# Kernel tuning notes

Hardware: AMD Instinct MI355X
Metric: run time of the kernel (lower is better)

Reference implementation:

```python
import jax, jax.numpy as jnp
import numpy as np

PATCH_SIZE = 128
IMG = 256


def _circle_perimeter(r_o, c_o, radius):
    # skimage.draw.circle_perimeter, method='bresenham' (midpoint circle),
    # including the duplicate octant-boundary points that skimage emits.
    rr, cc = [], []
    c, r = 0, radius
    d = 3 - 2 * radius
    while c <= r:
        rr += [r, -r, r, -r, c, -c, c, -c]
        cc += [c, c, -c, -c, r, r, -r, -r]
        if d < 0:
            d += 4 * c + 6
        else:
            d += 4 * (c - r) + 10
            r -= 1
        c += 1
    return np.asarray(rr) + r_o, np.asarray(cc) + c_o


def _radial_indices(patch_size, img):
    cy, cx = img // 2, img // 2
    rr_all, cc_all, seg_all = [], [], []
    for radius in range(1, patch_size - 1):  # radii 1..patch_size-2
        rr, cc = _circle_perimeter(cy, cx, radius)
        rr_all.append(rr)
        cc_all.append(cc)
        seg_all.append(np.full(rr.shape[0], radius - 1))
    return (np.concatenate(rr_all).astype(np.int32),
            np.concatenate(cc_all).astype(np.int32),
            np.concatenate(seg_all).astype(np.int32))


def setup_inputs() -> dict:
    key = jax.random.key(0)
    k1, k2 = jax.random.split(key)
    inp = jax.random.normal(k1, (64, 3, IMG, IMG), dtype=jnp.float32)
    tgt = jax.random.normal(k2, (64, 3, IMG, IMG), dtype=jnp.float32)
    w = np.float32(np.arange(0, 1, 1 / (PATCH_SIZE - 1)))  # length 127
    weights = jnp.asarray(w / np.sum(w))
    rr_idx, cc_idx, seg_ids = _radial_indices(PATCH_SIZE, IMG)
    return {"input": inp, "target": tgt, "weights": weights,
            "rr_idx": jnp.asarray(rr_idx), "cc_idx": jnp.asarray(cc_idx),
            "seg_ids": jnp.asarray(seg_ids)}


def reference(input, target, weights, rr_idx, cc_idx, seg_ids):
    B, C = input.shape[0], input.shape[1]
    R = weights.shape[0]          # patch_size - 1 curve bins
    nseg = R - 1                  # radii 1..patch_size-2
    f1 = jnp.fft.fft2(input)      # complex64 [B,C,H,W]
    f2 = jnp.fft.fft2(target)
    p1 = f1[:, :, rr_idx, cc_idx]  # [B,C,Ntot]
    p2 = f2[:, :, rr_idx, cc_idx]
    # original sums num/den over ALL dims (batch+channel+perimeter points)
    cross = jnp.sum(p1 * jnp.conj(p2), axis=(0, 1))        # [Ntot] complex
    pw1 = jnp.sum(jnp.abs(p1) ** 2, axis=(0, 1))           # [Ntot]
    pw2 = jnp.sum(jnp.abs(p2) ** 2, axis=(0, 1))
    num = jnp.abs(jax.ops.segment_sum(cross, seg_ids, num_segments=nseg))
    den = (jax.ops.segment_sum(pw1, seg_ids, num_segments=nseg) *
           jax.ops.segment_sum(pw2, seg_ids, num_segments=nseg))
    curve = jnp.concatenate([jnp.ones((1,), jnp.float32),
                             (num / jnp.sqrt(den)).astype(jnp.float32)])  # [R]
    # curve is identical across (b, c); Linear(R,1,bias=False) then total sum
    curve_full = jnp.broadcast_to(curve, (B, C, R))
    return jnp.sum(curve_full @ weights)
```

## Files before the change

### kernel.cpp

```cpp
#include <hip/hip_runtime.h>
#include <hip/hip_fp16.h>
#include <math.h>

#define NSEG 126

__device__ __forceinline__ unsigned bitrev8(unsigned v) { return __brev(v) >> 24; }

template <int K>
__device__ __forceinline__ void fftK(float2 x[][4], int lane) {
    const float PI = 3.14159265358979323846f;
    {
        float s, c;
        __sincosf(-PI * (float)lane * (1.0f / 128.0f), &s, &c);
        #pragma unroll
        for (int k = 0; k < K; k++) {
            float2 u, t, d;
            u = x[k][0]; t = x[k][2];
            x[k][0] = make_float2(u.x + t.x, u.y + t.y);
            d = make_float2(u.x - t.x, u.y - t.y);
            x[k][2] = make_float2(d.x * c - d.y * s, d.x * s + d.y * c);
            u = x[k][1]; t = x[k][3];
            x[k][1] = make_float2(u.x + t.x, u.y + t.y);
            d = make_float2(u.x - t.x, u.y - t.y);
            x[k][3] = make_float2(d.x * s + d.y * c, -d.x * c + d.y * s);
        }
    }
    {
        float s, c;
        __sincosf(-PI * (float)lane * (1.0f / 64.0f), &s, &c);
        #pragma unroll
        for (int k = 0; k < K; k++) {
            float2 u, t, d;
            u = x[k][0]; t = x[k][1];
            x[k][0] = make_float2(u.x + t.x, u.y + t.y);
            d = make_float2(u.x - t.x, u.y - t.y);
            x[k][1] = make_float2(d.x * c - d.y * s, d.x * s + d.y * c);
            u = x[k][2]; t = x[k][3];
            x[k][2] = make_float2(u.x + t.x, u.y + t.y);
            d = make_float2(u.x - t.x, u.y - t.y);
            x[k][3] = make_float2(d.x * c - d.y * s, d.x * s + d.y * c);
        }
    }
    #pragma unroll
    for (int hbit = 5; hbit >= 0; hbit--) {
        int h = 1 << hbit;
        int j = lane & (h - 1);
        float s, c;
        __sincosf(-PI * (float)j / (float)h, &s, &c);
        bool up = (lane & h) != 0;
        #pragma unroll
        for (int k = 0; k < K; k++) {
            #pragma unroll
            for (int i = 0; i < 4; i++) {
                float px = __shfl_xor(x[k][i].x, h);
                float py = __shfl_xor(x[k][i].y, h);
                if (up) {
                    float dx = px - x[k][i].x, dy = py - x[k][i].y;
                    x[k][i] = make_float2(dx * c - dy * s, dx * s + dy * c);
                } else {
                    x[k][i] = make_float2(x[k][i].x + px, x[k][i].y + py);
                }
            }
        }
    }
}

__global__ __launch_bounds__(1024) void prep_all(
    const int* __restrict__ rr, const int* __restrict__ cc,
    const int* __restrict__ seg, int n,
    int* __restrict__ starts, int* __restrict__ b_pack, float* __restrict__ acc)
{
    __shared__ int cnt[128];
    __shared__ int cur[128];
    int tid = threadIdx.x;
    if (tid < NSEG * 3) acc[tid] = 0.f;
    if (tid < 128) cnt[tid] = 0;
    __syncthreads();
    for (int i = tid; i < n; i += 1024) {
        int c = cc[i], r = rr[i];
        if ((c > 128) || (c == 128 && r > 128)) atomicAdd(&cnt[255 - c], 1);
    }
    __syncthreads();
    if (tid < 64) {
        int2 c2 = reinterpret_cast<const int2*>(cnt)[tid];
        int lsum = c2.x + c2.y;
        int pre = lsum;
        #pragma unroll
        for (int off = 1; off < 64; off <<= 1) {
            int v = __shfl_up(pre, off);
            if (tid >= off) pre += v;
        }
        int excl = pre - lsum;
        int2 outv = make_int2(excl, excl + c2.x);
        reinterpret_cast<int2*>(cur)[tid] = outv;
        reinterpret_cast<int2*>(starts)[tid] = outv;
        if (tid == 63) starts[128] = excl + c2.x + c2.y;
    }
    __syncthreads();
    for (int i = tid; i < n; i += 1024) {
        int c = cc[i], r = rr[i];
        if ((c > 128) || (c == 128 && r > 128)) {
            int j = 255 - c;
            int pos = atomicAdd(&cur[j], 1);
            int pr = (int)bitrev8((unsigned)r);
            int pm = (int)bitrev8((unsigned)(256 - r) & 255);
            b_pack[pos] = pr | (pm << 8) | (seg[i] << 16);
        }
    }
}

__global__ __launch_bounds__(512) void rowfft_kernel(
    const float* __restrict__ inp, const float* __restrict__ tgt,
    __half2* __restrict__ G, int pair_base)
{
    __shared__ float2 T[256 * 17];
    int bid    = blockIdx.x;
    int plocal = bid >> 4;
    int rowgrp = bid & 15;
    int wv     = threadIdx.x >> 6;
    int lane   = threadIdx.x & 63;
    size_t base = (((size_t)(pair_base + plocal)) << 16)
                + ((size_t)((rowgrp << 4) + (wv << 1)) << 8);
    const float* s1 = inp + base;
    const float* s2 = tgt + base;

    float2 x[2][4];
    #pragma unroll
    for (int k = 0; k < 2; k++)
        #pragma unroll
        for (int i = 0; i < 4; i++) {
            int e = (k << 8) + i * 64 + lane;
            x[k][i] = make_float2(s1[e], s2[e]);
        }
    fftK<2>(x, lane);

    #pragma unroll
    for (int k = 0; k < 2; k++)
        #pragma unroll
        for (int i = 0; i < 4; i++)
            T[(i * 64 + lane) * 17 + (wv << 1) + k] = x[k][i];
    __syncthreads();

    __half2* dst = G + (((size_t)plocal) << 16) + (rowgrp << 4);
    int xl = threadIdx.x & 15;
    int qb = threadIdx.x >> 4;
    #pragma unroll
    for (int ii = 0; ii < 8; ii++) {
        int q = qb + (ii << 5);
        float2 v = T[q * 17 + xl];
        dst[q * 256 + xl] = __float22half2_rn(v);
    }
}

__global__ __launch_bounds__(256) void colfft_gather_kernel(
    const __half2* __restrict__ G, const int* __restrict__ starts,
    const int* __restrict__ b_pack, float* __restrict__ acc)
{
    __shared__ float2 Fb[4][2][256];
    __shared__ float accl[NSEG * 3];
    int tid    = threadIdx.x;
    int wv     = tid >> 6;
    int lane   = tid & 63;
    int plocal = blockIdx.x >> 4;
    int b      = blockIdx.x & 15;
    int jbase  = (b << 3) + (wv << 1);

    for (int i = tid; i < NSEG * 3; i += 256) accl[i] = 0.f;
    __syncthreads();

    const __half2* Gp = G + (((size_t)plocal) << 16);
    int cols[4];
    cols[0] = jbase + 1;   cols[1] = 255 - jbase;
    cols[2] = jbase + 2;   cols[3] = 254 - jbase;

    __half2 h[4][4];
    #pragma unroll
    for (int k = 0; k < 4; k++) {
        int q = (int)bitrev8((unsigned)cols[k]);
        const __half2* col = Gp + ((size_t)q << 8);
        #pragma unroll
        for (int i = 0; i < 4; i++) h[k][i] = col[i * 64 + lane];
    }
    float2 x[4][4];
    #pragma unroll
    for (int k = 0; k < 4; k++)
        #pragma unroll
        for (int i = 0; i < 4; i++)
            x[k][i] = __half22float2(h[k][i]);

    fftK<4>(x, lane);

    float2* F_lo = &Fb[wv][0][0];
    float2* F_hi = &Fb[wv][1][0];
    #pragma unroll
    for (int kb = 0; kb < 2; kb++) {
        #pragma unroll
        for (int i = 0; i < 4; i++) {
            F_lo[i * 64 + lane] = x[2 * kb + 0][i];
            F_hi[i * 64 + lane] = x[2 * kb + 1][i];
        }
        int j = jbase + kb;
        int s0 = starts[j], s1 = starts[j + 1];
        int e  = s0 + lane;
        int pk = (e < s1) ? b_pack[e] : 0;
        while (e < s1) {
            int e2  = e + 64;
            int pk2 = (e2 < s1) ? b_pack[e2] : 0;
            float2 a = F_hi[pk & 255];
            float2 m = F_lo[(pk >> 8) & 255];
            int sg = pk >> 16;
            float f1x = a.x + m.x, f1y = a.y - m.y;
            float dx  = a.x - m.x, dy  = a.y + m.y;
            atomicAdd(&accl[sg * 3 + 0], f1x * dy - f1y * dx);
            atomicAdd(&accl[sg * 3 + 1], f1x * f1x + f1y * f1y);
            atomicAdd(&accl[sg * 3 + 2], dx * dx + dy * dy);
            e = e2; pk = pk2;
        }
    }
    __syncthreads();

    for (int i = tid; i < NSEG * 3; i += 256) {
        float v = accl[i];
        if (v != 0.f) atomicAdd(&acc[i], v);
    }
}

__global__ void final_kernel(const float* __restrict__ acc, const float* __restrict__ w,
                             float* __restrict__ out, float scale) {
    int lane = threadIdx.x;
    float val = 0.f;
    for (int s = lane; s < NSEG; s += 64) {
        float cr = acc[s * 3 + 0];
        float p1 = acc[s * 3 + 1];
        float p2 = acc[s * 3 + 2];
        float den = p1 * p2;
        float curve = den > 0.f ? fabsf(cr) * rsqrtf(den) : 0.f;
        val += curve * w[s + 1];
    }
    if (lane == 0) val += w[0];
    #pragma unroll
    for (int off = 32; off > 0; off >>= 1) val += __shfl_down(val, off);
    if (lane == 0) out[0] = scale * val;
}

extern "C" void kernel_launch(void* const* d_in, const int* in_sizes, int n_in,
                              void* d_out, int out_size, void* d_ws, size_t ws_size,
                              hipStream_t stream)
{
    const float* inp = (const float*)d_in[0];
    const float* tgt = (const float*)d_in[1];
    const float* wts = (const float*)d_in[2];
    const int*   rr  = (const int*)d_in[3];
    const int*   cc  = (const int*)d_in[4];
    const int*   sg  = (const int*)d_in[5];
    int npts   = in_sizes[3];
    int npairs = in_sizes[0] >> 16;

    char* ws = (char*)d_ws;
    float* acc    = (float*)(ws + 0);
    int*   starts = (int*)(ws + 2048);
    int*   b_pack = (int*)(ws + 4096);
    size_t goff = 4096 + (size_t)npts * 4;
    goff = (goff + 255) & ~(size_t)255;
    __half2* G = (__half2*)(ws + goff);

    size_t per_pair = (size_t)256 * 256 * sizeof(__half2);
    int maxchunk = (int)((ws_size > goff ? (ws_size - goff) : 0) / per_pair);
    if (maxchunk < 1) maxchunk = 1;
    if (maxchunk > npairs) maxchunk = npairs;

    prep_all<<<1, 1024, 0, stream>>>(rr, cc, sg, npts, starts, b_pack, acc);

    for (int pb = 0; pb < npairs; pb += maxchunk) {
        int cp = npairs - pb < maxchunk ? npairs - pb : maxchunk;
        rowfft_kernel<<<cp * 16, 512, 0, stream>>>(inp, tgt, G, pb);
        colfft_gather_kernel<<<cp * 16, 256, 0, stream>>>(G, starts, b_pack, acc);
    }

    final_kernel<<<1, 64, 0, stream>>>(acc, wts, (float*)d_out, (float)npairs);
}
```

Baseline: 236.4 us.

## Fuse row FFT, column FFT and gather into one LDS-resident kernel

Replaces the separate row-FFT and column-FFT+gather kernels, which exchanged a half-precision spectrum through global memory, with a single kernel per image pair and half-spectrum. Each block row-FFTs with float4 loads and a new shuffle-based radix schedule using constant twiddle steps, keeps only the 128 needed column bins transposed in LDS as half2, column-FFTs them in place, then gathers perimeter points straight from LDS. This removes the global round trip of the intermediate spectrum and the extra launches. In exchange, each block redoes every row FFT for both halves and uses a large LDS footprint, which lowers occupancy to about one block per CU.

```diff
diff --git a/kernel.cpp b/kernel.cpp
--- a/kernel.cpp
+++ b/kernel.cpp
@@ -3,15 +3,85 @@
 #include <math.h>
 
 #define NSEG 126
+#define PI_F 3.14159265358979323846f
+#define TLS 257
 
 __device__ __forceinline__ unsigned bitrev8(unsigned v) { return __brev(v) >> 24; }
+__device__ __forceinline__ unsigned bitrev6(unsigned v) { return __brev(v) >> 26; }
+__device__ __forceinline__ float2 cmulc(float2 a, float2 b) {
+    return make_float2(a.x*b.x - a.y*b.y, a.x*b.y + a.y*b.x);
+}
+__device__ __forceinline__ float2 mulmi(float2 a){ return make_float2(a.y, -a.x); }
+
+template <int K>
+__device__ __forceinline__ void stage_shfl(float2 x[][4], int lane, int hl,
+                                           float2 w0, float2 st1, float2 st2, float2 st3)
+{
+    float2 w1 = cmulc(w0, st1), w2 = cmulc(w0, st2), w3 = cmulc(w0, st3);
+    bool up = (lane & hl) != 0;
+    #pragma unroll
+    for (int k = 0; k < K; k++) {
+        #pragma unroll
+        for (int i = 0; i < 4; i++) {
+            float2 wi = (i == 0) ? w0 : (i == 1) ? w1 : (i == 2) ? w2 : w3;
+            float px = __shfl_xor(x[k][i].x, hl);
+            float py = __shfl_xor(x[k][i].y, hl);
+            if (up) {
+                float dx = px - x[k][i].x, dy = py - x[k][i].y;
+                x[k][i] = make_float2(dx*wi.x - dy*wi.y, dx*wi.y + dy*wi.x);
+            } else {
+                x[k][i] = make_float2(x[k][i].x + px, x[k][i].y + py);
+            }
+        }
+    }
+}
+
+template <int K>
+__device__ __forceinline__ void fft256_v2(float2 x[][4], int lane) {
+    { float s,c; __sincosf(-PI_F*(float)(lane&31)*(1.0f/32.0f), &s,&c);
+      stage_shfl<K>(x,lane,32, make_float2(c,s),
+        make_float2(0.99969882f,-0.02454123f),
+        make_float2(0.99879546f,-0.04906767f),
+        make_float2(0.99729046f,-0.07356456f)); }
+    { float s,c; __sincosf(-PI_F*(float)(lane&15)*(1.0f/16.0f), &s,&c);
+      stage_shfl<K>(x,lane,16, make_float2(c,s),
+        make_float2(0.99879546f,-0.04906767f),
+        make_float2(0.99518473f,-0.09801714f),
+        make_float2(0.98917651f,-0.14673047f)); }
+    { float s,c; __sincosf(-PI_F*(float)(lane&7)*(1.0f/8.0f), &s,&c);
+      stage_shfl<K>(x,lane,8, make_float2(c,s),
+        make_float2(0.99518473f,-0.09801714f),
+        make_float2(0.98078528f,-0.19509032f),
+        make_float2(0.95694034f,-0.29028468f)); }
+    { float s,c; __sincosf(-PI_F*(float)(lane&3)*(1.0f/4.0f), &s,&c);
+      stage_shfl<K>(x,lane,4, make_float2(c,s),
+        make_float2(0.98078528f,-0.19509032f),
+        make_float2(0.92387953f,-0.38268343f),
+        make_float2(0.83146961f,-0.55557023f)); }
+    { float2 w0 = (lane&1) ? make_float2(0.f,-1.f) : make_float2(1.f,0.f);
+      stage_shfl<K>(x,lane,2, w0,
+        make_float2(0.92387953f,-0.38268343f),
+        make_float2(0.70710678f,-0.70710678f),
+        make_float2(0.38268343f,-0.92387953f)); }
+    { stage_shfl<K>(x,lane,1, make_float2(1.f,0.f),
+        make_float2(0.70710678f,-0.70710678f),
+        make_float2(0.f,-1.f),
+        make_float2(-0.70710678f,-0.70710678f)); }
+    #pragma unroll
+    for (int k = 0; k < K; k++) {
+        float2 u, v;
+        u=x[k][0]; v=x[k][2]; x[k][0]=make_float2(u.x+v.x,u.y+v.y); x[k][2]=make_float2(u.x-v.x,u.y-v.y);
+        u=x[k][1]; v=x[k][3]; x[k][1]=make_float2(u.x+v.x,u.y+v.y); x[k][3]=mulmi(make_float2(u.x-v.x,u.y-v.y));
+        u=x[k][0]; v=x[k][1]; x[k][0]=make_float2(u.x+v.x,u.y+v.y); x[k][1]=make_float2(u.x-v.x,u.y-v.y);
+        u=x[k][2]; v=x[k][3]; x[k][2]=make_float2(u.x+v.x,u.y+v.y); x[k][3]=make_float2(u.x-v.x,u.y-v.y);
+    }
+}
 
 template <int K>
 __device__ __forceinline__ void fftK(float2 x[][4], int lane) {
-    const float PI = 3.14159265358979323846f;
     {
         float s, c;
-        __sincosf(-PI * (float)lane * (1.0f / 128.0f), &s, &c);
+        __sincosf(-PI_F * (float)lane * (1.0f / 128.0f), &s, &c);
         #pragma unroll
         for (int k = 0; k < K; k++) {
             float2 u, t, d;
@@ -27,7 +97,7 @@
     }
     {
         float s, c;
-        __sincosf(-PI * (float)lane * (1.0f / 64.0f), &s, &c);
+        __sincosf(-PI_F * (float)lane * (1.0f / 64.0f), &s, &c);
         #pragma unroll
         for (int k = 0; k < K; k++) {
             float2 u, t, d;
@@ -46,7 +116,7 @@
         int h = 1 << hbit;
         int j = lane & (h - 1);
         float s, c;
-        __sincosf(-PI * (float)j / (float)h, &s, &c);
+        __sincosf(-PI_F * (float)j / (float)h, &s, &c);
         bool up = (lane & h) != 0;
         #pragma unroll
         for (int k = 0; k < K; k++) {
@@ -102,126 +172,110 @@
         if ((c > 128) || (c == 128 && r > 128)) {
             int j = 255 - c;
             int pos = atomicAdd(&cur[j], 1);
-            int pr = (int)bitrev8((unsigned)r);
-            int pm = (int)bitrev8((unsigned)(256 - r) & 255);
-            b_pack[pos] = pr | (pm << 8) | (seg[i] << 16);
-        }
-    }
-}
-
-__global__ __launch_bounds__(512) void rowfft_kernel(
+            int sl, sh;
+            if (j < 64) { sl = j;      sh = 127 - j; }
+            else        { sl = j - 64; sh = 190 - j; }
+            b_pack[pos] = r | (sl << 8) | (sh << 15) | (seg[i] << 22);
+        }
+    }
+}
+
+__global__ __launch_bounds__(1024) void fused_kernel(
     const float* __restrict__ inp, const float* __restrict__ tgt,
-    __half2* __restrict__ G, int pair_base)
+    const int* __restrict__ starts, const int* __restrict__ b_pack,
+    float* __restrict__ acc)
 {
-    __shared__ float2 T[256 * 17];
-    int bid    = blockIdx.x;
-    int plocal = bid >> 4;
-    int rowgrp = bid & 15;
-    int wv     = threadIdx.x >> 6;
-    int lane   = threadIdx.x & 63;
-    size_t base = (((size_t)(pair_base + plocal)) << 16)
-                + ((size_t)((rowgrp << 4) + (wv << 1)) << 8);
-    const float* s1 = inp + base;
-    const float* s2 = tgt + base;
-
-    float2 x[2][4];
-    #pragma unroll
-    for (int k = 0; k < 2; k++)
-        #pragma unroll
-        for (int i = 0; i < 4; i++) {
-            int e = (k << 8) + i * 64 + lane;
-            x[k][i] = make_float2(s1[e], s2[e]);
-        }
-    fftK<2>(x, lane);
-
-    #pragma unroll
-    for (int k = 0; k < 2; k++)
-        #pragma unroll
-        for (int i = 0; i < 4; i++)
-            T[(i * 64 + lane) * 17 + (wv << 1) + k] = x[k][i];
-    __syncthreads();
-
-    __half2* dst = G + (((size_t)plocal) << 16) + (rowgrp << 4);
-    int xl = threadIdx.x & 15;
-    int qb = threadIdx.x >> 4;
-    #pragma unroll
-    for (int ii = 0; ii < 8; ii++) {
-        int q = qb + (ii << 5);
-        float2 v = T[q * 17 + xl];
-        dst[q * 256 + xl] = __float22half2_rn(v);
-    }
-}
-
-__global__ __launch_bounds__(256) void colfft_gather_kernel(
-    const __half2* __restrict__ G, const int* __restrict__ starts,
-    const int* __restrict__ b_pack, float* __restrict__ acc)
-{
-    __shared__ float2 Fb[4][2][256];
+    __shared__ __half2 Tl[128 * TLS];
     __shared__ float accl[NSEG * 3];
-    int tid    = threadIdx.x;
-    int wv     = tid >> 6;
-    int lane   = tid & 63;
-    int plocal = blockIdx.x >> 4;
-    int b      = blockIdx.x & 15;
-    int jbase  = (b << 3) + (wv << 1);
-
-    for (int i = tid; i < NSEG * 3; i += 256) accl[i] = 0.f;
-    __syncthreads();
-
-    const __half2* Gp = G + (((size_t)plocal) << 16);
-    int cols[4];
-    cols[0] = jbase + 1;   cols[1] = 255 - jbase;
-    cols[2] = jbase + 2;   cols[3] = 254 - jbase;
-
-    __half2 h[4][4];
-    #pragma unroll
-    for (int k = 0; k < 4; k++) {
-        int q = (int)bitrev8((unsigned)cols[k]);
-        const __half2* col = Gp + ((size_t)q << 8);
-        #pragma unroll
-        for (int i = 0; i < 4; i++) h[k][i] = col[i * 64 + lane];
-    }
-    float2 x[4][4];
-    #pragma unroll
-    for (int k = 0; k < 4; k++)
-        #pragma unroll
-        for (int i = 0; i < 4; i++)
-            x[k][i] = __half22float2(h[k][i]);
-
-    fftK<4>(x, lane);
-
-    float2* F_lo = &Fb[wv][0][0];
-    float2* F_hi = &Fb[wv][1][0];
-    #pragma unroll
-    for (int kb = 0; kb < 2; kb++) {
-        #pragma unroll
-        for (int i = 0; i < 4; i++) {
-            F_lo[i * 64 + lane] = x[2 * kb + 0][i];
-            F_hi[i * 64 + lane] = x[2 * kb + 1][i];
-        }
-        int j = jbase + kb;
-        int s0 = starts[j], s1 = starts[j + 1];
-        int e  = s0 + lane;
-        int pk = (e < s1) ? b_pack[e] : 0;
-        while (e < s1) {
-            int e2  = e + 64;
-            int pk2 = (e2 < s1) ? b_pack[e2] : 0;
-            float2 a = F_hi[pk & 255];
-            float2 m = F_lo[(pk >> 8) & 255];
-            int sg = pk >> 16;
-            float f1x = a.x + m.x, f1y = a.y - m.y;
-            float dx  = a.x - m.x, dy  = a.y + m.y;
-            atomicAdd(&accl[sg * 3 + 0], f1x * dy - f1y * dx);
-            atomicAdd(&accl[sg * 3 + 1], f1x * f1x + f1y * f1y);
-            atomicAdd(&accl[sg * 3 + 2], dx * dx + dy * dy);
-            e = e2; pk = pk2;
-        }
-    }
-    __syncthreads();
-
-    for (int i = tid; i < NSEG * 3; i += 256) {
-        float v = accl[i];
-        if (v != 0.f) atomicAdd(&acc[i], v);
+    int tid  = threadIdx.x;
+    int wv   = tid >> 6;
+    int lane = tid & 63;
+    int pair = blockIdx.x >> 1;
+    int h    = blockIdx.x & 1;
+
+    if (tid < NSEG * 3) accl[tid] = 0.f;
+
+    int b6 = (int)bitrev6((unsigned)lane);
+    size_t ibase = ((size_t)pair) << 16;
+
+    for (int rd = 0; rd < 4; rd++) {
+        int row0 = (rd << 6) + (wv << 2);
+        float2 x[4][4];
+        #pragma unroll
+        for (int k = 0; k < 4; k++) {
+            const float4* s1 = (const float4*)(inp + ibase + (size_t)(row0 + k) * 256);
+            const float4* s2 = (const float4*)(tgt + ibase + (size_t)(row0 + k) * 256);
+            float4 A = s1[lane], B = s2[lane];
+            x[k][0] = make_float2(A.x, B.x);
+            x[k][1] = make_float2(A.y, B.y);
+            x[k][2] = make_float2(A.z, B.z);
+            x[k][3] = make_float2(A.w, B.w);
+        }
+        fft256_v2<4>(x, lane);
+        #pragma unroll
+        for (int k = 0; k < 4; k++) {
+            int xr = row0 + k;
+            if (h == 0) {
+                if (b6 >= 1) Tl[(b6 - 1) * TLS + xr] = __float22half2_rn(x[k][0]);
+                else         Tl[63 * TLS + xr]       = __float22half2_rn(x[k][2]);
+                Tl[(64 + b6) * TLS + xr] = __float22half2_rn(x[k][3]);
+            } else {
+                if (b6 >= 1) Tl[(b6 - 1) * TLS + xr] = __float22half2_rn(x[k][2]);
+                Tl[(63 + b6) * TLS + xr] = __float22half2_rn(x[k][1]);
+            }
+        }
+    }
+    __syncthreads();
+
+    {
+        float2 y[8][4];
+        #pragma unroll
+        for (int k = 0; k < 8; k++) {
+            const __half2* src = Tl + (wv * 8 + k) * TLS;
+            #pragma unroll
+            for (int i = 0; i < 4; i++)
+                y[k][i] = __half22float2(src[i * 64 + lane]);
+        }
+        fftK<8>(y, lane);
+        #pragma unroll
+        for (int k = 0; k < 8; k++) {
+            __half2* dst = Tl + (wv * 8 + k) * TLS;
+            #pragma unroll
+            for (int i = 0; i < 4; i++)
+                dst[i * 64 + lane] = __float22half2_rn(y[k][i]);
+        }
+    }
+    __syncthreads();
+
+    int s64  = starts[64];
+    int sBeg = h ? s64 : 0;
+    int sEnd = h ? starts[128] : s64;
+    int e  = sBeg + tid;
+    int pk = (e < sEnd) ? b_pack[e] : 0;
+    while (e < sEnd) {
+        int e2  = e + 1024;
+        int pk2 = (e2 < sEnd) ? b_pack[e2] : 0;
+        int r  = pk & 255;
+        int sl = (pk >> 8) & 127;
+        int sh = (pk >> 15) & 127;
+        int sg = (pk >> 22) & 127;
+        int mr = (256 - r) & 255;
+        int pr = (int)bitrev8((unsigned)r);
+        int pm = (int)bitrev8((unsigned)mr);
+        float2 a = __half22float2(Tl[sh * TLS + pr]);
+        float2 m = __half22float2(Tl[sl * TLS + pm]);
+        float f1x = a.x + m.x, f1y = a.y - m.y;
+        float dx  = a.x - m.x, dy  = a.y + m.y;
+        atomicAdd(&accl[sg * 3 + 0], f1x * dy - f1y * dx);
+        atomicAdd(&accl[sg * 3 + 1], f1x * f1x + f1y * f1y);
+        atomicAdd(&accl[sg * 3 + 2], dx * dx + dy * dy);
+        e = e2; pk = pk2;
+    }
+    __syncthreads();
+
+    if (tid < NSEG * 3) {
+        float v = accl[tid];
+        if (v != 0.f) atomicAdd(&acc[tid], v);
     }
 }
 
@@ -260,22 +314,8 @@
     float* acc    = (float*)(ws + 0);
     int*   starts = (int*)(ws + 2048);
     int*   b_pack = (int*)(ws + 4096);
-    size_t goff = 4096 + (size_t)npts * 4;
-    goff = (goff + 255) & ~(size_t)255;
-    __half2* G = (__half2*)(ws + goff);
-
-    size_t per_pair = (size_t)256 * 256 * sizeof(__half2);
-    int maxchunk = (int)((ws_size > goff ? (ws_size - goff) : 0) / per_pair);
-    if (maxchunk < 1) maxchunk = 1;
-    if (maxchunk > npairs) maxchunk = npairs;
 
     prep_all<<<1, 1024, 0, stream>>>(rr, cc, sg, npts, starts, b_pack, acc);
-
-    for (int pb = 0; pb < npairs; pb += maxchunk) {
-        int cp = npairs - pb < maxchunk ? npairs - pb : maxchunk;
-        rowfft_kernel<<<cp * 16, 512, 0, stream>>>(inp, tgt, G, pb);
-        colfft_gather_kernel<<<cp * 16, 256, 0, stream>>>(G, starts, b_pack, acc);
-    }
-
+    fused_kernel<<<npairs * 2, 1024, 0, stream>>>(inp, tgt, starts, b_pack, acc);
     final_kernel<<<1, 64, 0, stream>>>(acc, wts, (float*)d_out, (float)npairs);
 }
```

Result: slower. 377.7 us (+59.8%).
